# Performance work log

Hardware: AMD Instinct MI355X
Metric: run time of the kernel (lower is better)

## Reference

```python
import jax, jax.numpy as jnp
import numpy as np

N, E, H, T = 50000, 100000, 512, 6  # nodes, edges, hidden_size, num_edge_types


def setup_inputs() -> dict:
    key = jax.random.key(0)
    ks = jax.random.split(key, 14)
    xav = 1.0 / np.sqrt(H)
    return {
        "statement_embeddings": jax.random.normal(ks[0], (N, H), jnp.float32),
        "source_indices": jax.random.randint(ks[1], (E,), 0, N, dtype=jnp.int32),
        "dest_indices": jax.random.randint(ks[2], (E,), 0, N, dtype=jnp.int32),
        "edge_types": jax.random.randint(ks[3], (E,), 0, T, dtype=jnp.int32),
        "num_nodes": N,
        "hidden_size": H,
        # edge_dense: Dense(features=6*H), xavier_uniform kernel, tiny-normal bias
        "W_edge": jax.random.uniform(ks[4], (H, T * H), jnp.float32, -1.0, 1.0) * np.sqrt(6.0 / (H + T * H)),
        "b_edge": jax.random.normal(ks[5], (T * H,), jnp.float32) * 1e-6,
        # GRUCell params (flax convention: input denses have bias; hidden r/z denses no bias; hidden n dense has bias)
        "W_ir": jax.random.normal(ks[6], (H, H), jnp.float32) * xav,
        "W_iz": jax.random.normal(ks[7], (H, H), jnp.float32) * xav,
        "W_in": jax.random.normal(ks[8], (H, H), jnp.float32) * xav,
        "b_ir": jnp.zeros((H,), jnp.float32),
        "b_iz": jnp.zeros((H,), jnp.float32),
        "b_in": jnp.zeros((H,), jnp.float32),
        "W_hr": jax.random.normal(ks[9], (H, H), jnp.float32) * xav,
        "W_hz": jax.random.normal(ks[10], (H, H), jnp.float32) * xav,
        "W_hn": jax.random.normal(ks[11], (H, H), jnp.float32) * xav,
        "b_hn": jnp.zeros((H,), jnp.float32),
    }


def reference(statement_embeddings, source_indices, dest_indices, edge_types,
              num_nodes, hidden_size,
              W_edge, b_edge,
              W_ir, W_iz, W_in, b_ir, b_iz, b_in,
              W_hr, W_hz, W_hn, b_hn):
    num_edge_types = 6
    # gather source node embeddings: [E, H]
    src = statement_embeddings[source_indices]
    # per-edge dense to all edge types: [E, T*H] -> [E, T, H]
    all_types = (src @ W_edge + b_edge).reshape(-1, num_edge_types, hidden_size)
    # select the slice for each edge's type: [E, H]
    msgs = jnp.take_along_axis(all_types, edge_types[:, None, None], axis=1)[:, 0, :]
    # scatter-add to destination nodes: [N, H]
    proposed = jax.ops.segment_sum(msgs, dest_indices, num_segments=num_nodes)
    # GRU update: inputs=proposed, carry=statement_embeddings
    h = statement_embeddings
    r = jax.nn.sigmoid(proposed @ W_ir + b_ir + h @ W_hr)
    z = jax.nn.sigmoid(proposed @ W_iz + b_iz + h @ W_hz)
    n = jnp.tanh(proposed @ W_in + b_in + r * (h @ W_hn + b_hn))
    return (1.0 - z) * n + z * h
```

## Files before the change

### kernel.cpp

```cpp
#include <hip/hip_runtime.h>
#include <hip/hip_bf16.h>
#include <math.h>

#define H 512
#define NT 6
#define BM 64
#define BN 64
#define BK 32
#define LDW (BK + 8)

typedef short bf16x8 __attribute__((ext_vector_type(8)));
typedef float f32x4 __attribute__((ext_vector_type(4)));

__device__ __forceinline__ float sigmoidf_(float x) { return 1.0f / (1.0f + expf(-x)); }

__device__ __forceinline__ unsigned short f2bf(float f) {
    unsigned int u = __float_as_uint(f);
    u = (u + 0x7FFF + ((u >> 16) & 1)) >> 16;
    return (unsigned short)u;
}

__global__ void hist_kernel(const int* __restrict__ etype, int E, int* __restrict__ meta) {
    __shared__ int lh[NT];
    if (threadIdx.x < NT) lh[threadIdx.x] = 0;
    __syncthreads();
    int i = blockIdx.x * blockDim.x + threadIdx.x;
    if (i < E) atomicAdd(&lh[etype[i]], 1);
    __syncthreads();
    if (threadIdx.x < NT) {
        int c = lh[threadIdx.x];
        if (c) atomicAdd(&meta[threadIdx.x], c);
    }
}

__global__ void prefix_kernel(int* __restrict__ meta) {
    if (threadIdx.x == 0 && blockIdx.x == 0) {
        int acc = 0;
        for (int t = 0; t < NT; ++t) {
            meta[8 + t]  = acc;
            meta[16 + t] = acc;
            acc += ((meta[t] + BM - 1) / BM) * BM;
        }
        meta[8 + NT] = acc;
    }
}

__global__ void scatter_perm_kernel(const int* __restrict__ etype, int E,
                                    int* __restrict__ meta, int* __restrict__ perm) {
    __shared__ int lcount[NT];
    __shared__ int lbase[NT];
    const int tid = threadIdx.x;
    if (tid < NT) lcount[tid] = 0;
    __syncthreads();
    int i = blockIdx.x * blockDim.x + tid;
    int t = 0, rank = 0;
    if (i < E) {
        t = etype[i];
        rank = atomicAdd(&lcount[t], 1);
    }
    __syncthreads();
    if (tid < NT) {
        int c = lcount[tid];
        lbase[tid] = c ? atomicAdd(&meta[16 + tid], c) : 0;
    }
    __syncthreads();
    if (i < E) perm[lbase[t] + rank] = i;
}

__global__ void conv_bf16_kernel(const float* __restrict__ in, unsigned short* __restrict__ out, int n4) {
    int i = blockIdx.x * blockDim.x + threadIdx.x;
    if (i < n4) {
        float4 v = ((const float4*)in)[i];
        ushort4 o;
        o.x = f2bf(v.x); o.y = f2bf(v.y); o.z = f2bf(v.z); o.w = f2bf(v.w);
        ((ushort4*)out)[i] = o;
    }
}

__global__ void conv_gru_w_kernel(const float* __restrict__ Wir, const float* __restrict__ Wiz,
                                  const float* __restrict__ Win, const float* __restrict__ Whr,
                                  const float* __restrict__ Whz, const float* __restrict__ Whn,
                                  unsigned short* __restrict__ Brt, unsigned short* __restrict__ Bzt,
                                  unsigned short* __restrict__ Bnit, unsigned short* __restrict__ Bnht) {
    int idx = blockIdx.x * blockDim.x + threadIdx.x;
    if (idx >= 512 * 1024) return;
    int n = idx >> 10;
    int k = idx & 1023;
    int kk = k & 511;
    const float* wr = (k < 512) ? Wir : Whr;
    const float* wz = (k < 512) ? Wiz : Whz;
    Brt[idx] = f2bf(wr[kk * H + n]);
    Bzt[idx] = f2bf(wz[kk * H + n]);
    if (k < 512) Bnit[n * H + k]  = f2bf(Win[k * H + n]);
    else         Bnht[n * H + kk] = f2bf(Whn[kk * H + n]);
}

__global__ void conv_edge_w_kernel(const float* __restrict__ W_edge, unsigned short* __restrict__ WeT) {
    int idx = blockIdx.x * blockDim.x + threadIdx.x;
    if (idx >= 3072 * 512) return;
    int n = idx >> 9;
    int k = idx & 511;
    WeT[idx] = f2bf(W_edge[(size_t)k * (NT * H) + n]);
}

__global__ __launch_bounds__(256)
void edge_msg_mfma(const unsigned short* __restrict__ emb_bf,
                   const int* __restrict__ src_idx,
                   const int* __restrict__ dst_idx,
                   const float* __restrict__ b_edge,
                   const unsigned short* __restrict__ WeT,
                   const int* __restrict__ meta,
                   const int* __restrict__ perm,
                   float* __restrict__ proposed)
{
    __shared__ short As[BM][LDW];
    __shared__ short Bs[BN][LDW];
    __shared__ int ls_src[BM];
    __shared__ int ls_dst[BM];

    const int rowBase = blockIdx.y * BM;
    if (rowBase >= meta[8 + NT]) return;
    int t = 0;
    while (rowBase >= meta[8 + t + 1]) ++t;

    const int colBase = blockIdx.x * BN;
    const int tid = threadIdx.x;

    if (tid < BM) {
        int e = perm[rowBase + tid];
        int s = -1, d = -1;
        if (e >= 0) { s = src_idx[e] * H; d = dst_idx[e] * H; }
        ls_src[tid] = s;
        ls_dst[tid] = d;
    }
    __syncthreads();

    const int sRow = tid >> 2;
    const int sK   = (tid & 3) * 8;
    const int lane = tid & 63;
    const int wave = tid >> 6;
    const int wm = (wave >> 1) * 32;
    const int wn = (wave & 1) * 32;
    const int q = lane >> 4;
    const int r = lane & 15;

    f32x4 acc[2][2];
    #pragma unroll
    for (int i = 0; i < 2; ++i)
        #pragma unroll
        for (int j = 0; j < 2; ++j) acc[i][j] = (f32x4){0.f, 0.f, 0.f, 0.f};

    const int sA = ls_src[sRow];
    const size_t bRowBase = ((size_t)(t * H + colBase + sRow)) * H;

    for (int k0 = 0; k0 < H; k0 += BK) {
        uint4 av = make_uint4(0, 0, 0, 0);
        if (sA >= 0) av = *(const uint4*)&emb_bf[(size_t)sA + k0 + sK];
        *(uint4*)&As[sRow][sK] = av;
        *(uint4*)&Bs[sRow][sK] = *(const uint4*)&WeT[bRowBase + k0 + sK];
        __syncthreads();
        #pragma unroll
        for (int i = 0; i < 2; ++i) {
            bf16x8 a = *(const bf16x8*)&As[wm + i * 16 + r][q * 8];
            #pragma unroll
            for (int j = 0; j < 2; ++j) {
                bf16x8 b = *(const bf16x8*)&Bs[wn + j * 16 + r][q * 8];
                acc[i][j] = __builtin_amdgcn_mfma_f32_16x16x32_bf16(a, b, acc[i][j], 0, 0, 0);
            }
        }
        __syncthreads();
    }

    #pragma unroll
    for (int i = 0; i < 2; ++i) {
        #pragma unroll
        for (int reg = 0; reg < 4; ++reg) {
            int rowL = wm + i * 16 + q * 4 + reg;
            int d = ls_dst[rowL];
            if (d < 0) continue;
            #pragma unroll
            for (int j = 0; j < 2; ++j) {
                int col = colBase + wn + j * 16 + r;
                atomicAdd(&proposed[(size_t)d + col], acc[i][j][reg] + b_edge[t * H + col]);
            }
        }
    }
}

__global__ __launch_bounds__(256)
void gru_mfma(const unsigned short* __restrict__ prop_bf,
              const unsigned short* __restrict__ emb_bf,
              const float* __restrict__ emb_f32,
              const unsigned short* __restrict__ Brt,
              const unsigned short* __restrict__ Bzt,
              const unsigned short* __restrict__ Bnit,
              const unsigned short* __restrict__ Bnht,
              const float* __restrict__ bir, const float* __restrict__ biz,
              const float* __restrict__ bin, const float* __restrict__ bhn,
              float* __restrict__ out, int N)
{
    __shared__ short As[BM][LDW];
    __shared__ short Brs[BN][LDW];
    __shared__ short Bzs[BN][LDW];
    __shared__ short Bns[BN][LDW];

    const int rowBase = blockIdx.y * BM;
    const int colBase = blockIdx.x * BN;
    const int tid = threadIdx.x;
    const int sRow = tid >> 2;
    const int sK   = (tid & 3) * 8;
    const int lane = tid & 63;
    const int wave = tid >> 6;
    const int wm = (wave >> 1) * 32;
    const int wn = (wave & 1) * 32;
    const int q = lane >> 4;
    const int r = lane & 15;

    const int aRow = rowBase + sRow;
    const bool aValid = aRow < N;

    f32x4 accR[2][2], accZ[2][2], accNI[2][2], accNH[2][2];
    #pragma unroll
    for (int i = 0; i < 2; ++i)
        #pragma unroll
        for (int j = 0; j < 2; ++j) {
            accR[i][j] = (f32x4){0.f, 0.f, 0.f, 0.f};
            accZ[i][j] = accR[i][j];
            accNI[i][j] = accR[i][j];
            accNH[i][j] = accR[i][j];
        }

    const size_t bRow = (size_t)(colBase + sRow);

    for (int k0 = 0; k0 < 2 * H; k0 += BK) {
        const bool half = (k0 >= H);
        const int kk = half ? (k0 - H) : k0;
        const unsigned short* Asrc = half ? emb_bf : prop_bf;
        uint4 av = make_uint4(0, 0, 0, 0);
        if (aValid) av = *(const uint4*)&Asrc[(size_t)aRow * H + kk + sK];
        *(uint4*)&As[sRow][sK] = av;
        *(uint4*)&Brs[sRow][sK] = *(const uint4*)&Brt[bRow * 1024 + k0 + sK];
        *(uint4*)&Bzs[sRow][sK] = *(const uint4*)&Bzt[bRow * 1024 + k0 + sK];
        const unsigned short* Bn = half ? Bnht : Bnit;
        *(uint4*)&Bns[sRow][sK] = *(const uint4*)&Bn[bRow * H + kk + sK];
        __syncthreads();

        #pragma unroll
        for (int i = 0; i < 2; ++i) {
            bf16x8 a = *(const bf16x8*)&As[wm + i * 16 + r][q * 8];
            #pragma unroll
            for (int j = 0; j < 2; ++j) {
                bf16x8 br = *(const bf16x8*)&Brs[wn + j * 16 + r][q * 8];
                bf16x8 bz = *(const bf16x8*)&Bzs[wn + j * 16 + r][q * 8];
                bf16x8 bn = *(const bf16x8*)&Bns[wn + j * 16 + r][q * 8];
                accR[i][j] = __builtin_amdgcn_mfma_f32_16x16x32_bf16(a, br, accR[i][j], 0, 0, 0);
                accZ[i][j] = __builtin_amdgcn_mfma_f32_16x16x32_bf16(a, bz, accZ[i][j], 0, 0, 0);
                if (half) accNH[i][j] = __builtin_amdgcn_mfma_f32_16x16x32_bf16(a, bn, accNH[i][j], 0, 0, 0);
                else      accNI[i][j] = __builtin_amdgcn_mfma_f32_16x16x32_bf16(a, bn, accNI[i][j], 0, 0, 0);
            }
        }
        __syncthreads();
    }

    #pragma unroll
    for (int i = 0; i < 2; ++i) {
        #pragma unroll
        for (int reg = 0; reg < 4; ++reg) {
            int row = rowBase + wm + i * 16 + q * 4 + reg;
            if (row >= N) continue;
            #pragma unroll
            for (int j = 0; j < 2; ++j) {
                int col = colBase + wn + j * 16 + r;
                float rg = sigmoidf_(accR[i][j][reg] + bir[col]);
                float zg = sigmoidf_(accZ[i][j][reg] + biz[col]);
                float ng = tanhf(accNI[i][j][reg] + bin[col] + rg * (accNH[i][j][reg] + bhn[col]));
                float h = emb_f32[(size_t)row * H + col];
                out[(size_t)row * H + col] = (1.0f - zg) * ng + zg * h;
            }
        }
    }
}

extern "C" void kernel_launch(void* const* d_in, const int* in_sizes, int n_in,
                              void* d_out, int out_size, void* d_ws, size_t ws_size,
                              hipStream_t stream) {
    const float* emb     = (const float*)d_in[0];
    const int*   src_idx = (const int*)d_in[1];
    const int*   dst_idx = (const int*)d_in[2];
    const int*   etype   = (const int*)d_in[3];
    const float* W_edge  = (const float*)d_in[6];
    const float* b_edge  = (const float*)d_in[7];
    const float* Wir = (const float*)d_in[8];
    const float* Wiz = (const float*)d_in[9];
    const float* Win = (const float*)d_in[10];
    const float* bir = (const float*)d_in[11];
    const float* biz = (const float*)d_in[12];
    const float* bin = (const float*)d_in[13];
    const float* Whr = (const float*)d_in[14];
    const float* Whz = (const float*)d_in[15];
    const float* Whn = (const float*)d_in[16];
    const float* bhn = (const float*)d_in[17];

    const int E = in_sizes[1];
    const int N = in_sizes[0] / H;
    const int NH = N * H;

    char* ws = (char*)d_ws;
    float*          proposed = (float*)ws;                       ws += (size_t)NH * 4;
    unsigned short* prop_bf  = (unsigned short*)ws;              ws += (size_t)NH * 2;
    unsigned short* emb_bf   = (unsigned short*)ws;              ws += (size_t)NH * 2;
    unsigned short* Brt      = (unsigned short*)ws;              ws += 512 * 1024 * 2;
    unsigned short* Bzt      = (unsigned short*)ws;              ws += 512 * 1024 * 2;
    unsigned short* Bnit     = (unsigned short*)ws;              ws += 512 * 512 * 2;
    unsigned short* Bnht     = (unsigned short*)ws;              ws += 512 * 512 * 2;
    unsigned short* WeT      = (unsigned short*)ws;              ws += 3072 * 512 * 2;
    int*            meta     = (int*)ws;                         ws += 32 * 4;
    int*            perm     = (int*)ws;
    const int maxRowTiles = (E + BM - 1) / BM + NT;

    hipMemsetAsync(proposed, 0, (size_t)NH * 4, stream);
    hipMemsetAsync(meta, 0, 32 * 4, stream);
    hipMemsetAsync(perm, 0xFF, (size_t)maxRowTiles * BM * 4, stream);

    const int n4 = NH / 4;
    conv_bf16_kernel<<<(n4 + 255) / 256, 256, 0, stream>>>(emb, emb_bf, n4);
    conv_gru_w_kernel<<<(512 * 1024 + 255) / 256, 256, 0, stream>>>(
        Wir, Wiz, Win, Whr, Whz, Whn, Brt, Bzt, Bnit, Bnht);
    conv_edge_w_kernel<<<(3072 * 512 + 255) / 256, 256, 0, stream>>>(W_edge, WeT);

    hist_kernel<<<(E + 255) / 256, 256, 0, stream>>>(etype, E, meta);
    prefix_kernel<<<1, 64, 0, stream>>>(meta);
    scatter_perm_kernel<<<(E + 255) / 256, 256, 0, stream>>>(etype, E, meta, perm);

    dim3 egrid(H / BN, maxRowTiles);
    edge_msg_mfma<<<egrid, 256, 0, stream>>>(emb_bf, src_idx, dst_idx, b_edge, WeT,
                                             meta, perm, proposed);

    conv_bf16_kernel<<<(n4 + 255) / 256, 256, 0, stream>>>(proposed, prop_bf, n4);

    dim3 ggrid(H / BN, (N + BM - 1) / BM);
    gru_mfma<<<ggrid, 256, 0, stream>>>(prop_bf, emb_bf, emb, Brt, Bzt, Bnit, Bnht,
                                        bir, biz, bin, bhn, (float*)d_out, N);
}
```

Baseline: 916.6 us.

## Enlarge MFMA tiles and load tiles directly to LDS in edge and GRU GEMMs

Both GEMM kernels move to 128-row tiles. The edge kernel uses 128x128 and the GRU kernel 128x64, so each wave accumulates a 4x4 or 4x2 grid of MFMA fragments and reuses operands more. Global-to-shared staging switches to global_load_lds 16-byte direct loads, and the GRU K-loop is split into two specialised halves. A workgroup index remap spreads GRU tiles across XCDs. The costs are higher register pressure, unpadded LDS rows that may cause bank conflicts, and unguarded A loads past N on the last GRU tile.

```diff
diff --git a/kernel.cpp b/kernel.cpp
--- a/kernel.cpp
+++ b/kernel.cpp
@@ -4,10 +4,13 @@
 
 #define H 512
 #define NT 6
-#define BM 64
-#define BN 64
-#define BK 32
-#define LDW (BK + 8)
+
+#define EBM 128
+#define EBN 128
+#define EBK 32
+#define GBM 128
+#define GBN 64
+#define GBK 32
 
 typedef short bf16x8 __attribute__((ext_vector_type(8)));
 typedef float f32x4 __attribute__((ext_vector_type(4)));
@@ -18,6 +21,12 @@
     unsigned int u = __float_as_uint(f);
     u = (u + 0x7FFF + ((u >> 16) & 1)) >> 16;
     return (unsigned short)u;
+}
+
+__device__ __forceinline__ void glds16(const void* g, void* l) {
+    __builtin_amdgcn_global_load_lds((const __attribute__((address_space(1))) unsigned int*)g,
+                                     (__attribute__((address_space(3))) unsigned int*)l,
+                                     16, 0, 0);
 }
 
 __global__ void hist_kernel(const int* __restrict__ etype, int E, int* __restrict__ meta) {
@@ -39,7 +48,7 @@
         for (int t = 0; t < NT; ++t) {
             meta[8 + t]  = acc;
             meta[16 + t] = acc;
-            acc += ((meta[t] + BM - 1) / BM) * BM;
+            acc += ((meta[t] + EBM - 1) / EBM) * EBM;
         }
         meta[8 + NT] = acc;
     }
@@ -113,76 +122,87 @@
                    const int* __restrict__ perm,
                    float* __restrict__ proposed)
 {
-    __shared__ short As[BM][LDW];
-    __shared__ short Bs[BN][LDW];
-    __shared__ int ls_src[BM];
-    __shared__ int ls_dst[BM];
-
-    const int rowBase = blockIdx.y * BM;
+    __shared__ short As[EBM * EBK];
+    __shared__ short Bs[EBN * EBK];
+    __shared__ int ls_src[EBM];
+    __shared__ int ls_dst[EBM];
+
+    const int rowBase = blockIdx.y * EBM;
     if (rowBase >= meta[8 + NT]) return;
     int t = 0;
     while (rowBase >= meta[8 + t + 1]) ++t;
 
-    const int colBase = blockIdx.x * BN;
+    const int colBase = blockIdx.x * EBN;
     const int tid = threadIdx.x;
 
-    if (tid < BM) {
+    if (tid < EBM) {
         int e = perm[rowBase + tid];
-        int s = -1, d = -1;
+        int s = 0, d = -1;
         if (e >= 0) { s = src_idx[e] * H; d = dst_idx[e] * H; }
         ls_src[tid] = s;
         ls_dst[tid] = d;
     }
     __syncthreads();
 
-    const int sRow = tid >> 2;
-    const int sK   = (tid & 3) * 8;
     const int lane = tid & 63;
     const int wave = tid >> 6;
-    const int wm = (wave >> 1) * 32;
-    const int wn = (wave & 1) * 32;
+    const int wm = (wave >> 1) * 64;
+    const int wn = (wave & 1) * 64;
     const int q = lane >> 4;
     const int r = lane & 15;
 
-    f32x4 acc[2][2];
-    #pragma unroll
-    for (int i = 0; i < 2; ++i)
-        #pragma unroll
-        for (int j = 0; j < 2; ++j) acc[i][j] = (f32x4){0.f, 0.f, 0.f, 0.f};
-
-    const int sA = ls_src[sRow];
-    const size_t bRowBase = ((size_t)(t * H + colBase + sRow)) * H;
-
-    for (int k0 = 0; k0 < H; k0 += BK) {
-        uint4 av = make_uint4(0, 0, 0, 0);
-        if (sA >= 0) av = *(const uint4*)&emb_bf[(size_t)sA + k0 + sK];
-        *(uint4*)&As[sRow][sK] = av;
-        *(uint4*)&Bs[sRow][sK] = *(const uint4*)&WeT[bRowBase + k0 + sK];
+    const int rA   = tid >> 2;
+    const int slot = (tid & 3) * 8;
+
+    const int s0 = ls_src[rA];
+    const int s1 = ls_src[64 + rA];
+    const size_t b0 = ((size_t)(t * H + colBase + rA)) * H + slot;
+    const size_t b1 = ((size_t)(t * H + colBase + 64 + rA)) * H + slot;
+
+    f32x4 acc[4][4];
+    #pragma unroll
+    for (int i = 0; i < 4; ++i)
+        #pragma unroll
+        for (int j = 0; j < 4; ++j) acc[i][j] = (f32x4){0.f, 0.f, 0.f, 0.f};
+
+    for (int k0 = 0; k0 < H; k0 += EBK) {
+        glds16(emb_bf + (size_t)s0 + k0 + slot, &As[tid * 8]);
+        glds16(emb_bf + (size_t)s1 + k0 + slot, &As[(256 + tid) * 8]);
+        glds16(WeT + b0 + k0, &Bs[tid * 8]);
+        glds16(WeT + b1 + k0, &Bs[(256 + tid) * 8]);
         __syncthreads();
-        #pragma unroll
-        for (int i = 0; i < 2; ++i) {
-            bf16x8 a = *(const bf16x8*)&As[wm + i * 16 + r][q * 8];
+
+        bf16x8 a[4];
+        #pragma unroll
+        for (int i = 0; i < 4; ++i)
+            a[i] = *(const bf16x8*)&As[(wm + i * 16 + r) * EBK + q * 8];
+        #pragma unroll
+        for (int j = 0; j < 4; ++j) {
+            bf16x8 b = *(const bf16x8*)&Bs[(wn + j * 16 + r) * EBK + q * 8];
             #pragma unroll
-            for (int j = 0; j < 2; ++j) {
-                bf16x8 b = *(const bf16x8*)&Bs[wn + j * 16 + r][q * 8];
-                acc[i][j] = __builtin_amdgcn_mfma_f32_16x16x32_bf16(a, b, acc[i][j], 0, 0, 0);
-            }
+            for (int i = 0; i < 4; ++i)
+                acc[i][j] = __builtin_amdgcn_mfma_f32_16x16x32_bf16(a[i], b, acc[i][j], 0, 0, 0);
         }
         __syncthreads();
     }
 
-    #pragma unroll
-    for (int i = 0; i < 2; ++i) {
+    int cols[4];
+    float bias[4];
+    #pragma unroll
+    for (int j = 0; j < 4; ++j) {
+        cols[j] = colBase + wn + j * 16 + r;
+        bias[j] = b_edge[t * H + cols[j]];
+    }
+    #pragma unroll
+    for (int i = 0; i < 4; ++i) {
         #pragma unroll
         for (int reg = 0; reg < 4; ++reg) {
-            int rowL = wm + i * 16 + q * 4 + reg;
-            int d = ls_dst[rowL];
+            int row = wm + i * 16 + q * 4 + reg;
+            int d = ls_dst[row];
             if (d < 0) continue;
             #pragma unroll
-            for (int j = 0; j < 2; ++j) {
-                int col = colBase + wn + j * 16 + r;
-                atomicAdd(&proposed[(size_t)d + col], acc[i][j][reg] + b_edge[t * H + col]);
-            }
+            for (int j = 0; j < 4; ++j)
+                atomicAdd(&proposed[(size_t)d + cols[j]], acc[i][j][reg] + bias[j]);
         }
     }
 }
@@ -199,29 +219,39 @@
               const float* __restrict__ bin, const float* __restrict__ bhn,
               float* __restrict__ out, int N)
 {
-    __shared__ short As[BM][LDW];
-    __shared__ short Brs[BN][LDW];
-    __shared__ short Bzs[BN][LDW];
-    __shared__ short Bns[BN][LDW];
-
-    const int rowBase = blockIdx.y * BM;
-    const int colBase = blockIdx.x * BN;
+    __shared__ short As[GBM * GBK];
+    __shared__ short Brs[GBN * GBK];
+    __shared__ short Bzs[GBN * GBK];
+    __shared__ short Bns[GBN * GBK];
+
+    int wg = blockIdx.y * gridDim.x + blockIdx.x;
+    const int nwg = gridDim.x * gridDim.y;
+    if ((nwg & 7) == 0) {
+        const int cpx = nwg >> 3;
+        wg = (wg & 7) * cpx + (wg >> 3);
+    }
+    const int rowBase = (wg / gridDim.x) * GBM;
+    const int colBase = (wg % gridDim.x) * GBN;
+
     const int tid = threadIdx.x;
-    const int sRow = tid >> 2;
-    const int sK   = (tid & 3) * 8;
     const int lane = tid & 63;
     const int wave = tid >> 6;
-    const int wm = (wave >> 1) * 32;
+    const int wm = (wave >> 1) * 64;
     const int wn = (wave & 1) * 32;
     const int q = lane >> 4;
     const int r = lane & 15;
 
-    const int aRow = rowBase + sRow;
-    const bool aValid = aRow < N;
-
-    f32x4 accR[2][2], accZ[2][2], accNI[2][2], accNH[2][2];
-    #pragma unroll
-    for (int i = 0; i < 2; ++i)
+    const int rA   = tid >> 2;
+    const int slot = (tid & 3) * 8;
+
+    const size_t aOff0  = (size_t)(rowBase + rA) * H + slot;
+    const size_t aOff1  = (size_t)(rowBase + 64 + rA) * H + slot;
+    const size_t bOffRZ = (size_t)(colBase + rA) * 1024 + slot;
+    const size_t bOffN  = (size_t)(colBase + rA) * 512 + slot;
+
+    f32x4 accR[4][2], accZ[4][2], accNI[4][2], accNH[4][2];
+    #pragma unroll
+    for (int i = 0; i < 4; ++i)
         #pragma unroll
         for (int j = 0; j < 2; ++j) {
             accR[i][j] = (f32x4){0.f, 0.f, 0.f, 0.f};
@@ -230,50 +260,52 @@
             accNH[i][j] = accR[i][j];
         }
 
-    const size_t bRow = (size_t)(colBase + sRow);
-
-    for (int k0 = 0; k0 < 2 * H; k0 += BK) {
-        const bool half = (k0 >= H);
-        const int kk = half ? (k0 - H) : k0;
-        const unsigned short* Asrc = half ? emb_bf : prop_bf;
-        uint4 av = make_uint4(0, 0, 0, 0);
-        if (aValid) av = *(const uint4*)&Asrc[(size_t)aRow * H + kk + sK];
-        *(uint4*)&As[sRow][sK] = av;
-        *(uint4*)&Brs[sRow][sK] = *(const uint4*)&Brt[bRow * 1024 + k0 + sK];
-        *(uint4*)&Bzs[sRow][sK] = *(const uint4*)&Bzt[bRow * 1024 + k0 + sK];
-        const unsigned short* Bn = half ? Bnht : Bnit;
-        *(uint4*)&Bns[sRow][sK] = *(const uint4*)&Bn[bRow * H + kk + sK];
-        __syncthreads();
-
-        #pragma unroll
-        for (int i = 0; i < 2; ++i) {
-            bf16x8 a = *(const bf16x8*)&As[wm + i * 16 + r][q * 8];
+#define GRU_STEP(ASRC, BNSRC, ACCN, K0, KK)                                                          \
+    {                                                                                                \
+        glds16(ASRC + aOff0 + (KK), &As[tid * 8]);                                                   \
+        glds16(ASRC + aOff1 + (KK), &As[(256 + tid) * 8]);                                           \
+        glds16(Brt + bOffRZ + (K0), &Brs[tid * 8]);                                                  \
+        glds16(Bzt + bOffRZ + (K0), &Bzs[tid * 8]);                                                  \
+        glds16(BNSRC + bOffN + (KK), &Bns[tid * 8]);                                                 \
+        __syncthreads();                                                                             \
+        bf16x8 a[4];                                                                                 \
+        _Pragma("unroll")                                                                            \
+        for (int i = 0; i < 4; ++i)                                                                  \
+            a[i] = *(const bf16x8*)&As[(wm + i * 16 + r) * GBK + q * 8];                             \
+        _Pragma("unroll")                                                                            \
+        for (int j = 0; j < 2; ++j) {                                                                \
+            bf16x8 br = *(const bf16x8*)&Brs[(wn + j * 16 + r) * GBK + q * 8];                       \
+            bf16x8 bz = *(const bf16x8*)&Bzs[(wn + j * 16 + r) * GBK + q * 8];                       \
+            bf16x8 bn = *(const bf16x8*)&Bns[(wn + j * 16 + r) * GBK + q * 8];                       \
+            _Pragma("unroll")                                                                        \
+            for (int i = 0; i < 4; ++i) {                                                            \
+                accR[i][j] = __builtin_amdgcn_mfma_f32_16x16x32_bf16(a[i], br, accR[i][j], 0, 0, 0); \
+                accZ[i][j] = __builtin_amdgcn_mfma_f32_16x16x32_bf16(a[i], bz, accZ[i][j], 0, 0, 0); \
+                ACCN[i][j] = __builtin_amdgcn_mfma_f32_16x16x32_bf16(a[i], bn, ACCN[i][j], 0, 0, 0); \
+            }                                                                                        \
+        }                                                                                            \
+        __syncthreads();                                                                             \
+    }
+
+    for (int k0 = 0; k0 < 512; k0 += GBK)
+        GRU_STEP(prop_bf, Bnit, accNI, k0, k0)
+    for (int k0 = 512; k0 < 1024; k0 += GBK)
+        GRU_STEP(emb_bf, Bnht, accNH, k0, k0 - 512)
+#undef GRU_STEP
+
+    #pragma unroll
+    for (int j = 0; j < 2; ++j) {
+        const int col = colBase + wn + j * 16 + r;
+        const float vbir = bir[col], vbiz = biz[col], vbin = bin[col], vbhn = bhn[col];
+        #pragma unroll
+        for (int i = 0; i < 4; ++i) {
             #pragma unroll
-            for (int j = 0; j < 2; ++j) {
-                bf16x8 br = *(const bf16x8*)&Brs[wn + j * 16 + r][q * 8];
-                bf16x8 bz = *(const bf16x8*)&Bzs[wn + j * 16 + r][q * 8];
-                bf16x8 bn = *(const bf16x8*)&Bns[wn + j * 16 + r][q * 8];
-                accR[i][j] = __builtin_amdgcn_mfma_f32_16x16x32_bf16(a, br, accR[i][j], 0, 0, 0);
-                accZ[i][j] = __builtin_amdgcn_mfma_f32_16x16x32_bf16(a, bz, accZ[i][j], 0, 0, 0);
-                if (half) accNH[i][j] = __builtin_amdgcn_mfma_f32_16x16x32_bf16(a, bn, accNH[i][j], 0, 0, 0);
-                else      accNI[i][j] = __builtin_amdgcn_mfma_f32_16x16x32_bf16(a, bn, accNI[i][j], 0, 0, 0);
-            }
-        }
-        __syncthreads();
-    }
-
-    #pragma unroll
-    for (int i = 0; i < 2; ++i) {
-        #pragma unroll
-        for (int reg = 0; reg < 4; ++reg) {
-            int row = rowBase + wm + i * 16 + q * 4 + reg;
-            if (row >= N) continue;
-            #pragma unroll
-            for (int j = 0; j < 2; ++j) {
-                int col = colBase + wn + j * 16 + r;
-                float rg = sigmoidf_(accR[i][j][reg] + bir[col]);
-                float zg = sigmoidf_(accZ[i][j][reg] + biz[col]);
-                float ng = tanhf(accNI[i][j][reg] + bin[col] + rg * (accNH[i][j][reg] + bhn[col]));
+            for (int reg = 0; reg < 4; ++reg) {
+                const int row = rowBase + wm + i * 16 + q * 4 + reg;
+                if (row >= N) continue;
+                float rg = sigmoidf_(accR[i][j][reg] + vbir);
+                float zg = sigmoidf_(accZ[i][j][reg] + vbiz);
+                float ng = tanhf(accNI[i][j][reg] + vbin + rg * (accNH[i][j][reg] + vbhn));
                 float h = emb_f32[(size_t)row * H + col];
                 out[(size_t)row * H + col] = (1.0f - zg) * ng + zg * h;
             }
@@ -316,11 +348,11 @@
     unsigned short* WeT      = (unsigned short*)ws;              ws += 3072 * 512 * 2;
     int*            meta     = (int*)ws;                         ws += 32 * 4;
     int*            perm     = (int*)ws;
-    const int maxRowTiles = (E + BM - 1) / BM + NT;
+    const int maxRowTiles = (E + EBM - 1) / EBM + NT;
 
     hipMemsetAsync(proposed, 0, (size_t)NH * 4, stream);
     hipMemsetAsync(meta, 0, 32 * 4, stream);
-    hipMemsetAsync(perm, 0xFF, (size_t)maxRowTiles * BM * 4, stream);
+    hipMemsetAsync(perm, 0xFF, (size_t)maxRowTiles * EBM * 4, stream);
 
     const int n4 = NH / 4;
     conv_bf16_kernel<<<(n4 + 255) / 256, 256, 0, stream>>>(emb, emb_bf, n4);
@@ -332,13 +364,13 @@
     prefix_kernel<<<1, 64, 0, stream>>>(meta);
     scatter_perm_kernel<<<(E + 255) / 256, 256, 0, stream>>>(etype, E, meta, perm);
 
-    dim3 egrid(H / BN, maxRowTiles);
+    dim3 egrid(H / EBN, maxRowTiles);
     edge_msg_mfma<<<egrid, 256, 0, stream>>>(emb_bf, src_idx, dst_idx, b_edge, WeT,
                                              meta, perm, proposed);
 
     conv_bf16_kernel<<<(n4 + 255) / 256, 256, 0, stream>>>(proposed, prop_bf, n4);
 
-    dim3 ggrid(H / BN, (N + BM - 1) / BM);
+    dim3 ggrid(H / GBN, (N + GBM - 1) / GBM);
     gru_mfma<<<ggrid, 256, 0, stream>>>(prop_bf, emb_bf, emb, Brt, Bzt, Bnit, Bnht,
                                         bir, biz, bin, bhn, (float*)d_out, N);
 }
```

New measurement: 1.068 ms. 16.6% more time.
